# Performance work log

Hardware: AMD Instinct MI355X
Metric: run time of the kernel (lower is better)

The kernel has to match this reference:

```python
import jax, jax.numpy as jnp
import numpy as np

D = 32            # dims[0] == dims[1] (modes per register)
K = 8             # kernel_size (filter interferometer modes)
STRIDE = 8        # stride (== kernel_size -> block-diagonal register)
N_BLOCKS = (D - K) // STRIDE + 1          # filters per register = 4
N_PHI = K * (K - 1) // 2                  # Reck triangle: one Ry BS per crossing = 28
BATCH = 16


def _filter_unitary(phi):
    """K-mode Reck-triangle interferometer of BS.Ry(theta=-2*phi) gates.
    Each gate mixes adjacent modes (j-1, j) with the real rotation
    [[cos phi, sin phi], [-sin phi, cos phi]]. Returns real [K, K] orthogonal."""
    U = jnp.eye(K, dtype=phi.dtype)
    idx = 0
    for i in range(1, K):
        for j in range(i, 0, -1):
            c, s = jnp.cos(phi[idx]), jnp.sin(phi[idx])
            r0 = c * U[j - 1] + s * U[j]
            r1 = -s * U[j - 1] + c * U[j]
            U = U.at[j - 1].set(r0).at[j].set(r1)
            idx += 1
    return U


def _register_unitary(phi):
    """D-mode register: the SAME filter unitary (shared params) placed every
    STRIDE modes; identity on any leftover modes. Block-diagonal [D, D]."""
    uf = _filter_unitary(phi)
    U = jnp.eye(D, dtype=phi.dtype)
    for b in range(N_BLOCKS):
        o = b * STRIDE
        U = U.at[o:o + K, o:o + K].set(uf)
    return U


def setup_inputs() -> dict:
    key = jax.random.key(0)
    k1, k2, k3 = jax.random.split(key, 3)
    two_pi = jnp.float32(2.0 * np.pi)
    return {
        "rho": jax.random.normal(k1, (BATCH, D * D, D * D), dtype=jnp.float32),
        "phi_x": two_pi * jax.random.uniform(k2, (N_PHI,), dtype=jnp.float32),
        "phi_y": two_pi * jax.random.uniform(k3, (N_PHI,), dtype=jnp.float32),
    }


def reference(rho, phi_x, phi_y):
    # u = kron(u_x, u_y) : [D^2, D^2] real orthogonal (BS circuit => real)
    u = jnp.kron(_register_unitary(phi_x), _register_unitary(phi_y))
    # new_rho = u @ rho @ u^dagger ; real => dagger is transpose
    u_rho = jnp.einsum('ij,bjk->bik', u, rho)   # [b, D^2, D^2]
    return u_rho @ u.T
```

## Files before the change

### kernel.cpp

```cpp
#include <hip/hip_runtime.h>
#include <hip/hip_bf16.h>
#include <math.h>


typedef __attribute__((ext_vector_type(8))) short short8_t;
typedef __attribute__((ext_vector_type(4))) float f32x4;

__global__ void setup_w(const float* __restrict__ phi_x,
                        const float* __restrict__ phi_y,
                        unsigned short* __restrict__ W) {
    __shared__ float U[2][64];
    const int t = threadIdx.x;
    if (t < 2) {
        const float* phi = (t == 0) ? phi_x : phi_y;
        float Um[8][8];
#pragma unroll
        for (int i = 0; i < 8; ++i)
#pragma unroll
            for (int j = 0; j < 8; ++j) Um[i][j] = (i == j) ? 1.0f : 0.0f;
        int idx = 0;
#pragma unroll
        for (int i = 1; i < 8; ++i) {
#pragma unroll
            for (int j = i; j >= 1; --j) {
                const float c = cosf(phi[idx]);
                const float s = sinf(phi[idx]);
#pragma unroll
                for (int m = 0; m < 8; ++m) {
                    const float a = Um[j - 1][m], b = Um[j][m];
                    Um[j - 1][m] = c * a + s * b;
                    Um[j][m]     = -s * a + c * b;
                }
                ++idx;
            }
        }
#pragma unroll
        for (int i = 0; i < 8; ++i)
#pragma unroll
            for (int j = 0; j < 8; ++j) U[t][i * 8 + j] = Um[i][j];
    }
    __syncthreads();
    const int xi = t >> 3, yi = t & 7;
#pragma unroll
    for (int j = 0; j < 64; ++j) {
        const int xj = j >> 3, yj = j & 7;
        const float w = U[0][xi * 8 + xj] * U[1][yi * 8 + yj];
        __hip_bfloat16 h = __float2bfloat16(w);
        W[t * 64 + j] = *reinterpret_cast<const unsigned short*>(&h);
    }
}

__device__ __forceinline__ unsigned short bf16bits(float v) {
    __hip_bfloat16 h = __float2bfloat16(v);
    return *reinterpret_cast<const unsigned short*>(&h);
}

__global__ __launch_bounds__(512) void qconv_mfma2(const float* __restrict__ rho,
                                                   const unsigned short* __restrict__ Wg,
                                                   float* __restrict__ out) {
    extern __shared__ __align__(16) unsigned short L[];
    const int t  = threadIdx.x;
    const int w  = t >> 6;
    const int l  = t & 63;

    const int bid = blockIdx.x;
    const int ch  = bid & 1;
    const int bi  = (bid >> 1) & 15;
    const int b   = bid >> 5;

    const int    rowb    = (bi >> 2) * 256 + (bi & 3) * 8;
    const size_t B0      = (size_t)b << 20;
    const int    colbase = ch * 512;

    {
        float4 v[16];
#pragma unroll
        for (int j = 0; j < 8; ++j) {
            const float* __restrict__ src =
                rho + B0 + (size_t)(rowb + w * 32 + j) * 1024 + colbase;
#pragma unroll
            for (int k2 = 0; k2 < 2; ++k2)
                v[j * 2 + k2] =
                    *reinterpret_cast<const float4*>(src + 4 * l + 256 * k2);
        }
#pragma unroll
        for (int j = 0; j < 8; ++j) {
            const int rt = 8 * w + j;
#pragma unroll
            for (int k2 = 0; k2 < 2; ++k2) {
                const int gc = 4 * l + 256 * k2;
                const int u     = ((gc >> 8) << 1) | ((gc >> 4) & 1);
                const int pcolc = ((gc >> 3) & 1) * 8 + ((gc >> 5) & 7);
                const int chunk = pcolc ^ (rt & 15);
                ushort4 h;
                const float4 x = v[j * 2 + k2];
                h.x = bf16bits(x.x); h.y = bf16bits(x.y);
                h.z = bf16bits(x.z); h.w = bf16bits(x.w);
                *reinterpret_cast<ushort4*>(
                    &L[u * 8192 + rt * 128 + (chunk << 3) + (gc & 7)]) = h;
            }
        }
    }
    __syncthreads();

    const int ln = l & 15;
    const int q  = l >> 4;
    const unsigned short* __restrict__ Tp = &L[(w >> 1) * 8192];
    unsigned short* __restrict__ Qs       = &L[32768 + w * 1024];
    const int wc = (w & 1) * 8;

    const int bx2 = 2 * ch + (w >> 2);
    const int by2 = w & 3;

#pragma unroll 1
    for (int m = 0; m < 4; ++m) {
        const short8_t AW0 = *reinterpret_cast<const short8_t*>(
            Wg + (16 * m + ln) * 64 + q * 8);
        const short8_t AW1 = *reinterpret_cast<const short8_t*>(
            Wg + (16 * m + ln) * 64 + 32 + q * 8);
        f32x4 acc[4];
#pragma unroll
        for (int tc = 0; tc < 4; ++tc) {
            const int prow = 16 * tc + ln;
            const short8_t BT0 = *reinterpret_cast<const short8_t*>(
                Tp + prow * 128 + (((wc + 0 + q) ^ (prow & 15)) << 3));
            const short8_t BT1 = *reinterpret_cast<const short8_t*>(
                Tp + prow * 128 + (((wc + 4 + q) ^ (prow & 15)) << 3));
            f32x4 c = {0.0f, 0.0f, 0.0f, 0.0f};
            c = __builtin_amdgcn_mfma_f32_16x16x32_bf16(AW0, BT0, c, 0, 0, 0);
            c = __builtin_amdgcn_mfma_f32_16x16x32_bf16(AW1, BT1, c, 0, 0, 0);
            acc[tc] = c;
        }

#pragma unroll
        for (int tc = 0; tc < 4; ++tc)
#pragma unroll
            for (int i = 0; i < 4; ++i) {
                const int qrow = 4 * q + i;
                const int qcol = 16 * tc + ln;
                Qs[qrow * 64 + (((qcol >> 3) ^ (qrow & 7)) << 3) + (qcol & 7)] =
                    bf16bits(acc[tc][i]);
            }

        const short8_t AQ0 = *reinterpret_cast<const short8_t*>(
            Qs + ln * 64 + (((0 + q) ^ (ln & 7)) << 3));
        const short8_t AQ1 = *reinterpret_cast<const short8_t*>(
            Qs + ln * 64 + (((4 + q) ^ (ln & 7)) << 3));
#pragma unroll
        for (int tc = 0; tc < 4; ++tc) {
            const short8_t BW0 = *reinterpret_cast<const short8_t*>(
                Wg + (16 * tc + ln) * 64 + q * 8);
            const short8_t BW1 = *reinterpret_cast<const short8_t*>(
                Wg + (16 * tc + ln) * 64 + 32 + q * 8);
            f32x4 o = {0.0f, 0.0f, 0.0f, 0.0f};
            o = __builtin_amdgcn_mfma_f32_16x16x32_bf16(AQ0, BW0, o, 0, 0, 0);
            o = __builtin_amdgcn_mfma_f32_16x16x32_bf16(AQ1, BW1, o, 0, 0, 0);

            const int grow = rowb + (2 * tc + (ln >> 3)) * 32 + (ln & 7);
            const int c0   = 16 * m + 4 * q;
            const int gcol = bx2 * 256 + (c0 >> 3) * 32 + by2 * 8 + (c0 & 7);
            *reinterpret_cast<float4*>(out + B0 + (size_t)grow * 1024 + gcol) =
                make_float4(o[0], o[1], o[2], o[3]);
        }
    }
}

extern "C" void kernel_launch(void* const* d_in, const int* in_sizes, int n_in,
                              void* d_out, int out_size, void* d_ws, size_t ws_size,
                              hipStream_t stream) {
    const float* rho   = (const float*)d_in[0];
    const float* phi_x = (const float*)d_in[1];
    const float* phi_y = (const float*)d_in[2];
    float* out = (float*)d_out;
    unsigned short* W = (unsigned short*)d_ws;

    setup_w<<<1, 64, 0, stream>>>(phi_x, phi_y, W);
    qconv_mfma2<<<512, 512, 81920, stream>>>(rho, W, out);
}
```

Before: 43.80 us.

## Split work into smaller 256-thread blocks with one column chunk each

```diff
diff --git a/kernel.cpp b/kernel.cpp
--- a/kernel.cpp
+++ b/kernel.cpp
@@ -55,50 +55,44 @@
     return *reinterpret_cast<const unsigned short*>(&h);
 }
 
-__global__ __launch_bounds__(512) void qconv_mfma2(const float* __restrict__ rho,
+__global__ __launch_bounds__(256) void qconv_mfma3(const float* __restrict__ rho,
                                                    const unsigned short* __restrict__ Wg,
                                                    float* __restrict__ out) {
     extern __shared__ __align__(16) unsigned short L[];
-    const int t  = threadIdx.x;
-    const int w  = t >> 6;
-    const int l  = t & 63;
+    const int t = threadIdx.x;
+    const int w = t >> 6;
+    const int l = t & 63;
 
-    const int bid = blockIdx.x;
-    const int ch  = bid & 1;
-    const int bi  = (bid >> 1) & 15;
-    const int b   = bid >> 5;
+    const int uid = blockIdx.x;
+    const int ch2 = uid & 3;
+    const int bi  = (uid >> 2) & 15;
+    const int b   = uid >> 6;
 
-    const int    rowb    = (bi >> 2) * 256 + (bi & 3) * 8;
-    const size_t B0      = (size_t)b << 20;
-    const int    colbase = ch * 512;
+    const size_t B0   = (size_t)b << 20;
+    const int    rowb = (bi >> 2) * 256 + (bi & 3) * 8;
+
+    const float* __restrict__ src = rho + B0 + ch2 * 256 + 4 * l;
+    float4 v[16];
+#pragma unroll
+    for (int j = 0; j < 16; ++j) {
+        const int rt   = j * 4 + w;
+        const int grow = rowb + (rt >> 3) * 32 + (rt & 7);
+        v[j] = *reinterpret_cast<const float4*>(src + (size_t)grow * 1024);
+    }
+    __builtin_amdgcn_sched_barrier(0);
 
     {
-        float4 v[16];
+        const int u0 = (l >> 2) & 1;
+        const int pc = ((l >> 1) & 1) * 8 + ((l >> 3) & 7);
+        const int el = (l & 1) * 4;
 #pragma unroll
-        for (int j = 0; j < 8; ++j) {
-            const float* __restrict__ src =
-                rho + B0 + (size_t)(rowb + w * 32 + j) * 1024 + colbase;
-#pragma unroll
-            for (int k2 = 0; k2 < 2; ++k2)
-                v[j * 2 + k2] =
-                    *reinterpret_cast<const float4*>(src + 4 * l + 256 * k2);
-        }
-#pragma unroll
-        for (int j = 0; j < 8; ++j) {
-            const int rt = 8 * w + j;
-#pragma unroll
-            for (int k2 = 0; k2 < 2; ++k2) {
-                const int gc = 4 * l + 256 * k2;
-                const int u     = ((gc >> 8) << 1) | ((gc >> 4) & 1);
-                const int pcolc = ((gc >> 3) & 1) * 8 + ((gc >> 5) & 7);
-                const int chunk = pcolc ^ (rt & 15);
-                ushort4 h;
-                const float4 x = v[j * 2 + k2];
-                h.x = bf16bits(x.x); h.y = bf16bits(x.y);
-                h.z = bf16bits(x.z); h.w = bf16bits(x.w);
-                *reinterpret_cast<ushort4*>(
-                    &L[u * 8192 + rt * 128 + (chunk << 3) + (gc & 7)]) = h;
-            }
+        for (int j = 0; j < 16; ++j) {
+            const int rt = j * 4 + w;
+            ushort4 h;
+            h.x = bf16bits(v[j].x); h.y = bf16bits(v[j].y);
+            h.z = bf16bits(v[j].z); h.w = bf16bits(v[j].w);
+            *reinterpret_cast<ushort4*>(
+                &L[(u0 * 64 + rt) * 128 + ((pc ^ (rt & 15)) << 3) + el]) = h;
         }
     }
     __syncthreads();
@@ -106,13 +100,11 @@
     const int ln = l & 15;
     const int q  = l >> 4;
     const unsigned short* __restrict__ Tp = &L[(w >> 1) * 8192];
-    unsigned short* __restrict__ Qs       = &L[32768 + w * 1024];
-    const int wc = (w & 1) * 8;
+    unsigned short* __restrict__ Qs       = &L[16384 + w * 1024];
+    const int wc  = (w & 1) * 8;
+    const int bx2 = ch2, by2 = w;
 
-    const int bx2 = 2 * ch + (w >> 2);
-    const int by2 = w & 3;
-
-#pragma unroll 1
+#pragma unroll
     for (int m = 0; m < 4; ++m) {
         const short8_t AW0 = *reinterpret_cast<const short8_t*>(
             Wg + (16 * m + ln) * 64 + q * 8);
@@ -175,5 +167,5 @@
     unsigned short* W = (unsigned short*)d_ws;
 
     setup_w<<<1, 64, 0, stream>>>(phi_x, phi_y, W);
-    qconv_mfma2<<<512, 512, 81920, stream>>>(rho, W, out);
+    qconv_mfma3<<<1024, 256, 40960, stream>>>(rho, W, out);
 }
```

Result: slower. 47.63 us (+8.7%).
